# Optimization experiments

Hardware: AMD Instinct MI355X
Metric: run time of the kernel (lower is better)

Reference implementation:

```python
import jax, jax.numpy as jnp
import numpy as np

# Faithful math of CustomAttn(method='tanh').forward:
#   E[i,j] = Linear_{4h->1}( tanh( concat(e_i, e_j) ) )
#          = w[:2h] . tanh(e_i) + w[2h:] . tanh(e_j) + b
#   out    = softmax(E, axis=0)
# Since tanh is elementwise and the linear layer is a dot product, the
# pairwise score decomposes into a_i + b_j + bias, computed with two
# O(n*d) matvecs and one broadcasted add (honoring the original math
# exactly while avoiding the O(n^2) python loop).

SEQ_LEN = 8192
HIDDEN = 256  # hidden_size; feature dim of encoder_outputs is 2*HIDDEN


def setup_inputs() -> dict:
    key = jax.random.key(0)
    k1, k2 = jax.random.split(key)
    encoder_outputs = jax.random.normal(k1, (SEQ_LEN, 2 * HIDDEN), dtype=jnp.float32)
    attn2_w = jax.random.normal(k2, (4 * HIDDEN,), dtype=jnp.float32) * (1.0 / np.sqrt(4 * HIDDEN))
    attn2_b = jnp.zeros((1,), dtype=jnp.float32)
    return {"encoder_outputs": encoder_outputs, "attn2_w": attn2_w, "attn2_b": attn2_b}


def reference(encoder_outputs, attn2_w, attn2_b):
    d = encoder_outputs.shape[1]  # 2*hidden_size
    t = jnp.tanh(encoder_outputs)            # [S, 2h]
    a = t @ attn2_w[:d]                      # [S], contribution of e_i
    b = t @ attn2_w[d:]                      # [S], contribution of e_j
    energies = a[:, None] + b[None, :] + attn2_b[0]  # [S, S]
    return jax.nn.softmax(energies, axis=0)
```

## Files before the change

kernel.cpp:

```cpp
#include <hip/hip_runtime.h>
#include <math.h>

#define SEQ 8192
#define DIM 512

typedef float floatx4 __attribute__((ext_vector_type(4)));

__global__ __launch_bounds__(256) void ca_exp_a(
    const float* __restrict__ e, const float* __restrict__ w,
    float* __restrict__ exp_a) {
    const int wave = threadIdx.x >> 6;
    const int lane = threadIdx.x & 63;
    const int row  = blockIdx.x * 4 + wave;
    const float* er = e + (size_t)row * DIM + lane * 8;
    const float* wr = w + lane * 8;

    float4 e0 = *reinterpret_cast<const float4*>(er);
    float4 e1 = *reinterpret_cast<const float4*>(er + 4);
    float4 w0 = *reinterpret_cast<const float4*>(wr);
    float4 w1 = *reinterpret_cast<const float4*>(wr + 4);

    float sum = tanhf(e0.x) * w0.x + tanhf(e0.y) * w0.y +
                tanhf(e0.z) * w0.z + tanhf(e0.w) * w0.w +
                tanhf(e1.x) * w1.x + tanhf(e1.y) * w1.y +
                tanhf(e1.z) * w1.z + tanhf(e1.w) * w1.w;

    #pragma unroll
    for (int off = 32; off; off >>= 1) sum += __shfl_down(sum, off, 64);
    if (lane == 0) exp_a[row] = expf(sum);
}

__global__ __launch_bounds__(1024) void ca_normalize(
    const float* __restrict__ exp_a, float* __restrict__ p) {
    __shared__ float red[16];
    const int tid = threadIdx.x;
    const floatx4* ev = reinterpret_cast<const floatx4*>(exp_a);
    floatx4 v0 = ev[tid * 2];
    floatx4 v1 = ev[tid * 2 + 1];
    float s = ((v0.x + v0.y) + (v0.z + v0.w)) +
              ((v1.x + v1.y) + (v1.z + v1.w));
    #pragma unroll
    for (int off = 32; off; off >>= 1) s += __shfl_down(s, off, 64);
    if ((tid & 63) == 0) red[tid >> 6] = s;
    __syncthreads();
    float S = 0.f;
    #pragma unroll
    for (int i = 0; i < 16; ++i) S += red[i];
    const float inv = 1.0f / S;
    floatx4 o0, o1;
    o0.x = v0.x * inv; o0.y = v0.y * inv; o0.z = v0.z * inv; o0.w = v0.w * inv;
    o1.x = v1.x * inv; o1.y = v1.y * inv; o1.z = v1.z * inv; o1.w = v1.w * inv;
    floatx4* pv = reinterpret_cast<floatx4*>(p);
    pv[tid * 2]     = o0;
    pv[tid * 2 + 1] = o1;
}

__global__ __launch_bounds__(256) void ca_bcast(
    const float* __restrict__ p, floatx4* __restrict__ out) {
    const int t = threadIdx.x;
    const int rbase = blockIdx.x * 32;
    float pv[32];
    #pragma unroll
    for (int r = 0; r < 32; ++r) pv[r] = p[rbase + r];
    #pragma unroll
    for (int r = 0; r < 32; ++r) {
        floatx4 f;
        f.x = pv[r]; f.y = pv[r]; f.z = pv[r]; f.w = pv[r];
        floatx4* o = out + (size_t)(rbase + r) * (SEQ / 4) + t;
        #pragma unroll
        for (int k = 0; k < 8; ++k) o[k * 256] = f;
    }
}

extern "C" void kernel_launch(void* const* d_in, const int* in_sizes, int n_in,
                              void* d_out, int out_size, void* d_ws, size_t ws_size,
                              hipStream_t stream) {
    const float* enc = (const float*)d_in[0];
    const float* w   = (const float*)d_in[1];
    float* out = (float*)d_out;

    float* exp_a = (float*)d_ws;
    float* p     = exp_a + SEQ;

    ca_exp_a<<<SEQ / 4, 256, 0, stream>>>(enc, w, exp_a);
    ca_normalize<<<1, 1024, 0, stream>>>(exp_a, p);
    ca_bcast<<<256, 256, 0, stream>>>(p, (floatx4*)out);
}
```

Before: 55.72 us.

## Fuse softmax normalization into exp and broadcast kernels, dropping one launch

```diff
diff --git a/kernel.cpp b/kernel.cpp
--- a/kernel.cpp
+++ b/kernel.cpp
@@ -8,7 +8,8 @@
 
 __global__ __launch_bounds__(256) void ca_exp_a(
     const float* __restrict__ e, const float* __restrict__ w,
-    float* __restrict__ exp_a) {
+    float* __restrict__ exp_a, float* __restrict__ partials) {
+    __shared__ float exps[4];
     const int wave = threadIdx.x >> 6;
     const int lane = threadIdx.x & 63;
     const int row  = blockIdx.x * 4 + wave;
@@ -27,41 +28,39 @@
 
     #pragma unroll
     for (int off = 32; off; off >>= 1) sum += __shfl_down(sum, off, 64);
-    if (lane == 0) exp_a[row] = expf(sum);
+    if (lane == 0) {
+        const float ex = expf(sum);
+        exp_a[row] = ex;
+        exps[wave] = ex;
+    }
+    __syncthreads();
+    if (threadIdx.x == 0)
+        partials[blockIdx.x] = (exps[0] + exps[1]) + (exps[2] + exps[3]);
 }
 
-__global__ __launch_bounds__(1024) void ca_normalize(
-    const float* __restrict__ exp_a, float* __restrict__ p) {
-    __shared__ float red[16];
-    const int tid = threadIdx.x;
-    const floatx4* ev = reinterpret_cast<const floatx4*>(exp_a);
-    floatx4 v0 = ev[tid * 2];
-    floatx4 v1 = ev[tid * 2 + 1];
+__global__ __launch_bounds__(256) void ca_bcast(
+    const float* __restrict__ exp_a, const float* __restrict__ partials,
+    floatx4* __restrict__ out) {
+    __shared__ float red[4];
+    const int t    = threadIdx.x;
+    const int lane = t & 63;
+    const int wv   = t >> 6;
+
+    const floatx4* pvts = reinterpret_cast<const floatx4*>(partials);
+    floatx4 v0 = pvts[t * 2];
+    floatx4 v1 = pvts[t * 2 + 1];
     float s = ((v0.x + v0.y) + (v0.z + v0.w)) +
               ((v1.x + v1.y) + (v1.z + v1.w));
     #pragma unroll
     for (int off = 32; off; off >>= 1) s += __shfl_down(s, off, 64);
-    if ((tid & 63) == 0) red[tid >> 6] = s;
+    if (lane == 0) red[wv] = s;
     __syncthreads();
-    float S = 0.f;
-    #pragma unroll
-    for (int i = 0; i < 16; ++i) S += red[i];
-    const float inv = 1.0f / S;
-    floatx4 o0, o1;
-    o0.x = v0.x * inv; o0.y = v0.y * inv; o0.z = v0.z * inv; o0.w = v0.w * inv;
-    o1.x = v1.x * inv; o1.y = v1.y * inv; o1.z = v1.z * inv; o1.w = v1.w * inv;
-    floatx4* pv = reinterpret_cast<floatx4*>(p);
-    pv[tid * 2]     = o0;
-    pv[tid * 2 + 1] = o1;
-}
+    const float inv = 1.0f / ((red[0] + red[1]) + (red[2] + red[3]));
 
-__global__ __launch_bounds__(256) void ca_bcast(
-    const float* __restrict__ p, floatx4* __restrict__ out) {
-    const int t = threadIdx.x;
     const int rbase = blockIdx.x * 32;
     float pv[32];
     #pragma unroll
-    for (int r = 0; r < 32; ++r) pv[r] = p[rbase + r];
+    for (int r = 0; r < 32; ++r) pv[r] = exp_a[rbase + r] * inv;
     #pragma unroll
     for (int r = 0; r < 32; ++r) {
         floatx4 f;
@@ -79,10 +78,9 @@
     const float* w   = (const float*)d_in[1];
     float* out = (float*)d_out;
 
-    float* exp_a = (float*)d_ws;
-    float* p     = exp_a + SEQ;
+    float* exp_a    = (float*)d_ws;
+    float* partials = exp_a + SEQ;
 
-    ca_exp_a<<<SEQ / 4, 256, 0, stream>>>(enc, w, exp_a);
-    ca_normalize<<<1, 1024, 0, stream>>>(exp_a, p);
-    ca_bcast<<<256, 256, 0, stream>>>(p, (floatx4*)out);
+    ca_exp_a<<<SEQ / 4, 256, 0, stream>>>(enc, w, exp_a, partials);
+    ca_bcast<<<256, 256, 0, stream>>>(exp_a, partials, (floatx4*)out);
 }
```

New measurement: 53.67 us. 1.04x faster.
